# Kernel tuning notes

Hardware: AMD Instinct MI355X
Metric: run time of the kernel (lower is better)

## Reference

```python
import jax, jax.numpy as jnp
import numpy as np

N_QUBITS = 8
N_CYCLES = 4
B = 8192
C64 = jnp.complex64

# ---- gate matrices ----

def _ry_batched(t):  # t: [B] -> [B,2,2]
    c = jnp.cos(t / 2).astype(C64)
    s = jnp.sin(t / 2).astype(C64)
    return jnp.stack([jnp.stack([c, -s], -1), jnp.stack([s, c], -1)], -2)


def _rz_batched(p):  # p: [B] -> [B,2,2]
    e0 = jnp.exp(-0.5j * p.astype(C64))
    e1 = jnp.exp(0.5j * p.astype(C64))
    z = jnp.zeros_like(e0)
    return jnp.stack([jnp.stack([e0, z], -1), jnp.stack([z, e1], -1)], -2)


def _rx(t):  # scalar -> [2,2]
    c = jnp.cos(t / 2).astype(C64)
    s = (-1j * jnp.sin(t / 2)).astype(C64)
    return jnp.stack([jnp.stack([c, s]), jnp.stack([s, c])])


def _crx(t):  # scalar -> [4,4] block-diag(I2, RX(t)), control = first index
    return jnp.eye(4, dtype=C64).at[2:, 2:].set(_rx(t))


def _u3(t, p, l):  # scalars -> [2,2]
    ct = jnp.cos(t / 2).astype(C64)
    st = jnp.sin(t / 2).astype(C64)
    eil = jnp.exp(1j * l.astype(C64))
    eip = jnp.exp(1j * p.astype(C64))
    return jnp.stack([jnp.stack([ct, -eil * st]), jnp.stack([eip * st, eip * eil * ct])])

CNOT = jnp.array([[1, 0, 0, 0], [0, 1, 0, 0], [0, 0, 0, 1], [0, 0, 1, 0]], dtype=C64)

# ---- statevector ops (state: [B] + [2]*N_QUBITS) ----

def apply_1q(state, U, wire):
    b = state.shape[0]
    s = jnp.moveaxis(state, 1 + wire, 1).reshape(b, 2, -1)
    s = jnp.einsum('bij,bjk->bik', U, s) if U.ndim == 3 else jnp.einsum('ij,bjk->bik', U, s)
    return jnp.moveaxis(s.reshape((b,) + (2,) * N_QUBITS), 1, 1 + wire)


def apply_2q(state, U, wc, wt):
    b = state.shape[0]
    s = jnp.moveaxis(state, (1 + wc, 1 + wt), (1, 2)).reshape(b, 4, -1)
    s = jnp.einsum('ij,bjk->bik', U, s)
    return jnp.moveaxis(s.reshape((b,) + (2,) * N_QUBITS), (1, 2), (1 + wc, 1 + wt))


def expval_z(state, wire):  # <Z_wire> : [B]
    probs = state.real ** 2 + state.imag ** 2
    axes = tuple(a for a in range(1, N_QUBITS + 1) if a != 1 + wire)
    z = jnp.sum(probs, axis=axes)  # [B,2]
    return z[:, 0] - z[:, 1]


def _circuit(theta, phi, crx_params, u3_params):
    b = theta.shape[0]
    state = jnp.zeros((b, 2 ** N_QUBITS), dtype=C64).at[:, 0].set(1.0)
    state = state.reshape((b,) + (2,) * N_QUBITS)
    # circuit builder: RY(theta), RZ(phi) on every wire + CNOT ring, n_cycles times
    U = jnp.einsum('bij,bjk->bik', _rz_batched(phi), _ry_batched(theta))  # RZ @ RY, [B,2,2]
    for _ in range(N_CYCLES):
        for w in range(N_QUBITS):
            state = apply_1q(state, U, w)
        for w in range(N_QUBITS):
            state = apply_2q(state, CNOT, w, (w + 1) % N_QUBITS)
    # QCNN layer 1
    for i, (c, t) in enumerate([(0, 1), (2, 3), (4, 5), (6, 7), (1, 2), (3, 4), (5, 6)]):
        state = apply_2q(state, _crx(crx_params[i]), c, t)
    # (intermediate expvals on [0,2,4,6] are computed then discarded in original)
    for i, w in enumerate([1, 3, 5, 7]):
        p = u3_params[i]
        state = apply_1q(state, _u3(p[0], p[1], p[2]), w)
    for i, (c, t) in enumerate([(1, 3), (5, 7), (3, 5)]):
        state = apply_2q(state, _crx(crx_params[7 + i]), c, t)
    for i, w in enumerate([3, 7]):
        p = u3_params[4 + i]
        state = apply_1q(state, _u3(p[0], p[1], p[2]), w)
    state = apply_2q(state, _crx(crx_params[10]), 3, 7)
    p = u3_params[6]
    state = apply_1q(state, _u3(p[0], p[1], p[2]), 7)
    ev = expval_z(state, 7)[:, None]  # [B,1]
    return jax.nn.relu(ev)


def setup_inputs() -> dict:
    key = jax.random.key(0)
    k1, k2, k3, k4 = jax.random.split(key, 4)
    two_pi = 2.0 * np.pi
    return {
        'theta': jax.random.uniform(k1, (B,), jnp.float32, 0.0, two_pi),
        'phi': jax.random.uniform(k2, (B,), jnp.float32, 0.0, two_pi),
        'crx_params': jax.random.uniform(k3, (11,), jnp.float32, 0.0, two_pi),
        'u3_params': jax.random.uniform(k4, (7, 3), jnp.float32, 0.0, two_pi),
    }


def reference(theta, phi, crx_params, u3_params):
    return _circuit(theta, phi, crx_params, u3_params)
```

## Files before the change

kernel.cpp:

```cpp
#include <hip/hip_runtime.h>
#include <math.h>


typedef float v2f __attribute__((ext_vector_type(2)));

__device__ __forceinline__ v2f pkmul(v2f a, v2f b) {
  v2f d; asm("v_pk_mul_f32 %0, %1, %2" : "=v"(d) : "v"(a), "v"(b)); return d;
}
__device__ __forceinline__ v2f pkfma(v2f a, v2f b, v2f c) {
  v2f d; asm("v_pk_fma_f32 %0, %1, %2, %3" : "=v"(d) : "v"(a), "v"(b), "v"(c)); return d;
}
__device__ __forceinline__ v2f pkmul_lo1(v2f a, v2f b) {
  v2f d; asm("v_pk_mul_f32 %0, %1, %2 op_sel:[0,0] op_sel_hi:[1,0]"
             : "=v"(d) : "v"(a), "v"(b)); return d;
}
__device__ __forceinline__ v2f pkfma_lo1(v2f a, v2f b, v2f c) {
  v2f d; asm("v_pk_fma_f32 %0, %1, %2, %3 op_sel:[0,0,0] op_sel_hi:[1,0,1]"
             : "=v"(d) : "v"(a), "v"(b), "v"(c)); return d;
}
__device__ __forceinline__ v2f pkfma_hi1(v2f a, v2f b, v2f c) {
  v2f d; asm("v_pk_fma_f32 %0, %1, %2, %3 op_sel:[0,1,0] op_sel_hi:[1,1,1]"
             : "=v"(d) : "v"(a), "v"(b), "v"(c)); return d;
}
__device__ __forceinline__ v2f pkfma_sw1(v2f a, v2f b, v2f c) {
  v2f d; asm("v_pk_fma_f32 %0, %1, %2, %3 op_sel:[0,1,0] op_sel_hi:[1,0,1]"
             : "=v"(d) : "v"(a), "v"(b), "v"(c)); return d;
}
__device__ __forceinline__ v2f dup(float x) { return (v2f){x, x}; }

template <int M>
__device__ __forceinline__ float shxm(float v) {
  if constexpr (M == 1 || M == 2 || M == 3 || M == 7 || M == 8 || M == 15) {
    constexpr int ctrl = (M == 1) ? 0xB1 : (M == 2) ? 0x4E : (M == 3) ? 0x1B
                         : (M == 7) ? 0x141 : (M == 8) ? 0x128 : 0x140;
    return __int_as_float(__builtin_amdgcn_update_dpp(
        0, __float_as_int(v), ctrl, 0xF, 0xF, true));
  } else {
    return __int_as_float(__builtin_amdgcn_ds_swizzle(
        __float_as_int(v), (M << 10) | 0x1F));
  }
}
template <int M>
__device__ __forceinline__ v2f shf2(v2f a) {
  return (v2f){shxm<M>(a.x), shxm<M>(a.y)};
}

struct G1 { float r00, i00, r01, i01, r10, i10, r11, i11; };

__device__ __forceinline__ void cplx_fma(v2f& R, v2f& I, v2f PR, v2f PI,
                                         v2f cAr, v2f cAi, v2f cAiN,
                                         v2f cBr, v2f cBi, v2f cBiN) {
  v2f NR = pkfma(cBiN, PI, pkfma(cBr, PR, pkfma(cAiN, I, pkmul(cAr, R))));
  v2f NI = pkfma(cBi, PR, pkfma(cBr, PI, pkfma(cAi, R, pkmul(cAr, I))));
  R = NR; I = NI;
}

__device__ __forceinline__ void apply_pair(v2f& LR, v2f& LI, v2f& HR, v2f& HI,
                                           float g00r, float g00i, float g01r,
                                           float g01i, float g10r, float g10i,
                                           float g11r, float g11i) {
  const v2f a00r = dup(g00r), a00i = dup(g00i), n00i = dup(-g00i);
  const v2f a01r = dup(g01r), a01i = dup(g01i), n01i = dup(-g01i);
  const v2f a10r = dup(g10r), a10i = dup(g10i), n10i = dup(-g10i);
  const v2f a11r = dup(g11r), a11i = dup(g11i), n11i = dup(-g11i);
  v2f NLR = pkfma(n01i, HI, pkfma(a01r, HR, pkfma(n00i, LI, pkmul(a00r, LR))));
  v2f NLI = pkfma(a01i, HR, pkfma(a01r, HI, pkfma(a00i, LR, pkmul(a00r, LI))));
  v2f NHR = pkfma(n11i, HI, pkfma(a11r, HR, pkfma(n10i, LI, pkmul(a10r, LR))));
  v2f NHI = pkfma(a11i, HR, pkfma(a11r, HI, pkfma(a10i, LR, pkmul(a10r, LI))));
  LR = NLR; LI = NLI; HR = NHR; HI = NHI;
}

__device__ __forceinline__ void crx_pairv(v2f& LR, v2f& LI, v2f& HR, v2f& HI,
                                          v2f cCC, v2f cSS, v2f cSSN) {
  v2f NLR = pkfma(cSS, HI, pkmul(cCC, LR));
  v2f NLI = pkfma(cSSN, HR, pkmul(cCC, LI));
  v2f NHR = pkfma(cSS, LI, pkmul(cCC, HR));
  v2f NHI = pkfma(cSSN, LR, pkmul(cCC, HI));
  LR = NLR; LI = NLI; HR = NHR; HI = NHI;
}

template <int RL, int VL>
__device__ __forceinline__ void u_lane(v2f (&CR)[4], v2f (&CI)[4], int l,
                                       float uAr, float uBi, float uAip,
                                       float uBrp) {
  const bool hi = (__popc(l & RL) & 1) != 0;
  const float Ai = hi ? uAip : -uAip;
  const float Br = hi ? uBrp : -uBrp;
  const v2f cAr = dup(uAr), cAi = dup(Ai), cAiN = dup(-Ai);
  const v2f cBr = dup(Br), cBi = dup(uBi), cBiN = dup(-uBi);
  v2f PR[4], PI[4];
#pragma unroll
  for (int q = 0; q < 4; ++q) { PR[q] = shf2<VL>(CR[q]); PI[q] = shf2<VL>(CI[q]); }
#pragma unroll
  for (int q = 0; q < 4; ++q)
    cplx_fma(CR[q], CI[q], PR[q], PI[q], cAr, cAi, cAiN, cBr, cBi, cBiN);
}

__device__ __forceinline__ void gate_pack(v2f (&CR)[4], v2f (&CI)[4],
                                          v2f cA, v2f cB, v2f cBn,
                                          v2f cC, v2f cD, v2f cDn) {
#pragma unroll
  for (int q = 0; q < 4; ++q) {
    v2f NR = pkfma_hi1(cDn, CI[q], pkfma_hi1(cC, CR[q],
             pkfma_lo1(cBn, CI[q], pkmul_lo1(cA, CR[q]))));
    v2f NI = pkfma_hi1(cD, CR[q], pkfma_hi1(cC, CI[q],
             pkfma_lo1(cB, CR[q], pkmul_lo1(cA, CI[q]))));
    CR[q] = NR; CI[q] = NI;
  }
}

__device__ __forceinline__ void u_reg4(v2f (&CR)[4], v2f (&CI)[4], float uAr,
                                       float uBi, float uAip, float uBrp) {
  gate_pack(CR, CI,
            (v2f){uAr, uBrp},
            (v2f){-uAip, uBi},
            (v2f){uAip, -uBi},
            (v2f){-uBrp, uAr},
            (v2f){uBi, uAip},
            (v2f){-uBi, -uAip});
}

__device__ __forceinline__ void u3_reg4(v2f (&CR)[4], v2f (&CI)[4], const G1& g) {
  gate_pack(CR, CI,
            (v2f){g.r00, g.r10},
            (v2f){g.i00, g.i10},
            (v2f){-g.i00, -g.i10},
            (v2f){g.r01, g.r11},
            (v2f){g.i01, g.i11},
            (v2f){-g.i01, -g.i11});
}

template <int RL>
__device__ __forceinline__ void cnot_lr4(v2f (&CR)[4], v2f (&CI)[4], int l) {
  const bool c = (__popc(l & RL) & 1) != 0;
#pragma unroll
  for (int q = 0; q < 4; ++q) {
    const float ax = CR[q].x, ay = CR[q].y;
    CR[q] = (v2f){c ? ay : ax, c ? ax : ay};
    const float bx = CI[q].x, by = CI[q].y;
    CI[q] = (v2f){c ? by : bx, c ? bx : by};
  }
}

__device__ __forceinline__ void cnot_swap42(v2f (&CR)[4], v2f (&CI)[4]) {
  float t;
  t = CR[0].y; CR[0].y = CR[2].y; CR[2].y = t;
  t = CR[1].y; CR[1].y = CR[3].y; CR[3].y = t;
  t = CI[0].y; CI[0].y = CI[2].y; CI[2].y = t;
  t = CI[1].y; CI[1].y = CI[3].y; CI[3].y = t;
}

__device__ __forceinline__ void cnot_swap21(v2f (&CR)[4], v2f (&CI)[4]) {
  v2f t;
  t = CR[2]; CR[2] = CR[3]; CR[3] = t;
  t = CI[2]; CI[2] = CI[3]; CI[3] = t;
}

template <int VL>
__device__ __forceinline__ void cnot_rl(v2f (&CR)[4], v2f (&CI)[4]) {
  CR[1] = shf2<VL>(CR[1]); CI[1] = shf2<VL>(CI[1]);
  CR[3] = shf2<VL>(CR[3]); CI[3] = shf2<VL>(CI[3]);
}

template <int RL, int VL>
__device__ __forceinline__ void crx_ll(v2f (&CR)[4], v2f (&CI)[4], int l,
                                       float co, float si) {
  const bool c = (__popc(l & RL) & 1) != 0;
  const float cc = c ? co : 1.f, ss = c ? si : 0.f;
  const v2f cCC = dup(cc), cSS = dup(ss), cSSN = dup(-ss);
  v2f PR[4], PI[4];
#pragma unroll
  for (int q = 0; q < 4; ++q) { PR[q] = shf2<VL>(CR[q]); PI[q] = shf2<VL>(CI[q]); }
#pragma unroll
  for (int q = 0; q < 4; ++q) {
    CR[q] = pkfma(cSS, PI[q], pkmul(cCC, CR[q]));
    CI[q] = pkfma(cSSN, PR[q], pkmul(cCC, CI[q]));
  }
}

template <int RL>
__device__ __forceinline__ void crx_lr4(v2f (&CR)[4], v2f (&CI)[4], int l,
                                        float co, float si) {
  const bool c = (__popc(l & RL) & 1) != 0;
  const float cc = c ? co : 1.f, ss = c ? si : 0.f;
  const v2f cc2 = dup(cc), ss2 = dup(ss), ssN2 = dup(-ss);
#pragma unroll
  for (int q = 0; q < 4; ++q) {
    v2f NR = pkfma_sw1(ss2, CI[q], pkmul(cc2, CR[q]));
    v2f NI = pkfma_sw1(ssN2, CR[q], pkmul(cc2, CI[q]));
    CR[q] = NR; CI[q] = NI;
  }
}

template <int RL, int VL>
__device__ __forceinline__ void u3_lane(v2f (&CR)[4], v2f (&CI)[4], int l,
                                        const G1& g) {
  const bool hi = (__popc(l & RL) & 1) != 0;
  const float Ar = hi ? g.r11 : g.r00, Aii = hi ? g.i11 : g.i00;
  const float Br = hi ? g.r10 : g.r01, Bi = hi ? g.i10 : g.i01;
  const v2f cAr = dup(Ar), cAi = dup(Aii), cAiN = dup(-Aii);
  const v2f cBr = dup(Br), cBi = dup(Bi), cBiN = dup(-Bi);
  v2f PR[4], PI[4];
#pragma unroll
  for (int q = 0; q < 4; ++q) { PR[q] = shf2<VL>(CR[q]); PI[q] = shf2<VL>(CI[q]); }
#pragma unroll
  for (int q = 0; q < 4; ++q)
    cplx_fma(CR[q], CI[q], PR[q], PI[q], cAr, cAi, cAiN, cBr, cBi, cBiN);
}

__device__ __forceinline__ G1 load_g1(const float* __restrict__ cs, int k) {
  const float* p = cs + 22 + 8 * k;
  G1 g;
  g.r00 = p[0]; g.i00 = p[1]; g.r01 = p[2]; g.i01 = p[3];
  g.r10 = p[4]; g.i10 = p[5]; g.r11 = p[6]; g.i11 = p[7];
  return g;
}

__global__ void prep_kernel(const float* __restrict__ crx,
                            const float* __restrict__ u3p,
                            float* __restrict__ ws) {
  const int t = threadIdx.x;
  if (t < 11) {
    float s, c;
    sincosf(0.5f * crx[t], &s, &c);
    ws[2 * t] = c; ws[2 * t + 1] = s;
  } else if (t >= 16 && t < 23) {
    const int k = t - 16;
    float st, ct, sp, cp, sl, cl;
    sincosf(0.5f * u3p[3 * k], &st, &ct);
    sincosf(u3p[3 * k + 1], &sp, &cp);
    sincosf(u3p[3 * k + 2], &sl, &cl);
    float* o = ws + 22 + 8 * k;
    o[0] = ct;            o[1] = 0.f;
    o[2] = -cl * st;      o[3] = -sl * st;
    o[4] = cp * st;       o[5] = sp * st;
    o[6] = (cp * cl - sp * sl) * ct;
    o[7] = (sp * cl + cp * sl) * ct;
  }
}

__global__ __launch_bounds__(256, 4) void qcnn_kernel(
    const float* __restrict__ theta, const float* __restrict__ phi,
    const float* __restrict__ cs, float* __restrict__ out, int nbatch) {
  const int tid = blockIdx.x * blockDim.x + threadIdx.x;
  const int wave = tid >> 6;
  const int lane = threadIdx.x & 63;
  const int l = lane & 31;
  int b = wave * 2 + (lane >> 5);
  if (b >= nbatch) b = nbatch - 1;

  v2f CR[4], CI[4];
#pragma unroll
  for (int q = 0; q < 4; ++q) { CR[q] = dup(0.f); CI[q] = dup(0.f); }
  if (l == 0) CR[0].x = 1.f;

  const float th = theta[b], ph = phi[b];
  float sth, cth, sph, cph;
  __sincosf(0.5f * th, &sth, &cth);
  __sincosf(0.5f * ph, &sph, &cph);
  const float uAr = cph * cth, uBi = sph * sth;
  const float uAip = sph * cth, uBrp = cph * sth;

#define ULANE(RL, VL) u_lane<RL, VL>(CR, CI, l, uAr, uBi, uAip, uBrp)
#define UPAIR(a, b_) apply_pair(CR[a], CI[a], CR[b_], CI[b_], uAr, -uAip, \
                                -uBrp, uBi, uBrp, uBi, uAr, uAip)
#define UREGS() do { u_reg4(CR, CI, uAr, uBi, uAip, uBrp); \
                     UPAIR(0, 2); UPAIR(1, 3); \
                     UPAIR(0, 1); UPAIR(2, 3); } while (0)
#define RING(RL45, VL70) do { cnot_lr4<RL45>(CR, CI, l); \
                              cnot_swap42(CR, CI); cnot_swap21(CR, CI); \
                              cnot_rl<VL70>(CR, CI); } while (0)

  ULANE(16, 16); ULANE(8, 8);   ULANE(4, 4);   ULANE(2, 2);  ULANE(1, 1);
  UREGS(); RING(31, 24);
  ULANE(16, 24); ULANE(24, 12); ULANE(28, 6);  ULANE(30, 3); ULANE(31, 1);
  UREGS(); RING(21, 20);
  ULANE(16, 20); ULANE(8, 10);  ULANE(20, 5);  ULANE(10, 2); ULANE(21, 1);
  UREGS(); RING(19, 30);
  ULANE(16, 30); ULANE(24, 15); ULANE(12, 7);  ULANE(6, 3);  ULANE(19, 1);
  UREGS(); RING(17, 17);
#undef RING
#undef UREGS
#undef UPAIR
#undef ULANE

#define LD(k) const float co##k = cs[2 * k], si##k = cs[2 * k + 1]
  LD(0); crx_ll<16, 8>(CR, CI, l, co0, si0);
  LD(1); crx_ll<4, 2>(CR, CI, l, co1, si1);
  LD(2); crx_lr4<17>(CR, CI, l, co2, si2);
  LD(3);
  crx_pairv(CR[2], CI[2], CR[3], CI[3], dup(co3), dup(si3), dup(-si3));
  LD(4); crx_ll<8, 4>(CR, CI, l, co4, si4);
  LD(5); crx_ll<2, 1>(CR, CI, l, co5, si5);
  LD(6);
  {
    const v2f cCC = (v2f){1.f, co6}, cSS = (v2f){0.f, si6}, cSSN = (v2f){0.f, -si6};
    crx_pairv(CR[0], CI[0], CR[2], CI[2], cCC, cSS, cSSN);
    crx_pairv(CR[1], CI[1], CR[3], CI[3], cCC, cSS, cSSN);
  }

  { G1 g = load_g1(cs, 0); u3_lane<8, 8>(CR, CI, l, g); }
  { G1 g = load_g1(cs, 1); u3_lane<2, 2>(CR, CI, l, g); }
  { G1 g = load_g1(cs, 2); u3_reg4(CR, CI, g); }
  { G1 g = load_g1(cs, 3);
    apply_pair(CR[0], CI[0], CR[1], CI[1], g.r00, g.i00, g.r01, g.i01,
               g.r10, g.i10, g.r11, g.i11);
    apply_pair(CR[2], CI[2], CR[3], CI[3], g.r00, g.i00, g.r01, g.i01,
               g.r10, g.i10, g.r11, g.i11); }

  LD(7); crx_ll<8, 2>(CR, CI, l, co7, si7);
  LD(8);
  {
    const v2f cCC = (v2f){1.f, co8}, cSS = (v2f){0.f, si8}, cSSN = (v2f){0.f, -si8};
    crx_pairv(CR[0], CI[0], CR[1], CI[1], cCC, cSS, cSSN);
    crx_pairv(CR[2], CI[2], CR[3], CI[3], cCC, cSS, cSSN);
  }
  LD(9); crx_lr4<2>(CR, CI, l, co9, si9);

  { G1 g = load_g1(cs, 4); u3_lane<2, 2>(CR, CI, l, g); }
  { G1 g = load_g1(cs, 5);
    apply_pair(CR[0], CI[0], CR[1], CI[1], g.r00, g.i00, g.r01, g.i01,
               g.r10, g.i10, g.r11, g.i11);
    apply_pair(CR[2], CI[2], CR[3], CI[3], g.r00, g.i00, g.r01, g.i01,
               g.r10, g.i10, g.r11, g.i11); }

  LD(10);
  {
    const bool c = (__popc(l & 2) & 1) != 0;
    const float cc = c ? co10 : 1.f, ss = c ? si10 : 0.f;
    const v2f cCC = dup(cc), cSS = dup(ss), cSSN = dup(-ss);
    crx_pairv(CR[0], CI[0], CR[1], CI[1], cCC, cSS, cSSN);
    crx_pairv(CR[2], CI[2], CR[3], CI[3], cCC, cSS, cSSN);
  }

  { G1 g = load_g1(cs, 6);
    apply_pair(CR[0], CI[0], CR[1], CI[1], g.r00, g.i00, g.r01, g.i01,
               g.r10, g.i10, g.r11, g.i11);
    apply_pair(CR[2], CI[2], CR[3], CI[3], g.r00, g.i00, g.r01, g.i01,
               g.r10, g.i10, g.r11, g.i11); }
#undef LD

  v2f S0 = pkfma(CI[0], CI[0], pkmul(CR[0], CR[0]));
  v2f S1 = pkfma(CI[1], CI[1], pkmul(CR[1], CR[1]));
  v2f S2 = pkfma(CI[2], CI[2], pkmul(CR[2], CR[2]));
  v2f S3 = pkfma(CI[3], CI[3], pkmul(CR[3], CR[3]));
  const v2f T = (S0 + S2) - (S1 + S3);
  float v = T.x + T.y;
  v += shxm<1>(v); v += shxm<2>(v); v += shxm<4>(v);
  v += shxm<8>(v); v += shxm<16>(v);
  if (l == 0) out[b] = fmaxf(v, 0.f);
}

extern "C" void kernel_launch(void* const* d_in, const int* in_sizes, int n_in,
                              void* d_out, int out_size, void* d_ws, size_t ws_size,
                              hipStream_t stream) {
  const float* theta = (const float*)d_in[0];
  const float* phi = (const float*)d_in[1];
  const float* crx = (const float*)d_in[2];
  const float* u3p = (const float*)d_in[3];
  float* out = (float*)d_out;
  float* ws = (float*)d_ws;
  const int nb = in_sizes[0];

  prep_kernel<<<1, 64, 0, stream>>>(crx, u3p, ws);

  const int elems_per_block = 8;
  dim3 block(256);
  dim3 grid((nb + elems_per_block - 1) / elems_per_block);
  qcnn_kernel<<<grid, block, 0, stream>>>(theta, phi, ws, out, nb);
}
```

Measured before the change: 78.18 us.

## Map each batch element to a full 64-lane wave with 4 amplitudes per lane

Changes the statevector split so a whole wave64 holds one batch element, each lane keeping 4 complex amplitudes instead of 8 across a half-wave. Gates on the extra qubit now run across lanes, using __shfl_xor for the 32-lane distance. Hand-written packed-FMA inline asm is replaced by compiler builtins (elementwise fma, shufflevector). Launch bounds go to 8 waves per SIMD and blocks to 4 elements. The intent is lower register pressure and higher occupancy, paid for with more cross-lane shuffles, including a slower cross-half shuffle, and twice as many waves.

```diff
diff --git a/kernel.cpp b/kernel.cpp
--- a/kernel.cpp
+++ b/kernel.cpp
@@ -4,27 +4,11 @@
 
 typedef float v2f __attribute__((ext_vector_type(2)));
 
-__device__ __forceinline__ v2f pkmul(v2f a, v2f b) {
-  v2f d; asm("v_pk_mul_f32 %0, %1, %2" : "=v"(d) : "v"(a), "v"(b)); return d;
-}
-__device__ __forceinline__ v2f pkfma(v2f a, v2f b, v2f c) {
-  v2f d; asm("v_pk_fma_f32 %0, %1, %2, %3" : "=v"(d) : "v"(a), "v"(b), "v"(c)); return d;
-}
-__device__ __forceinline__ v2f pkmul_lo1(v2f a, v2f b) {
-  v2f d; asm("v_pk_mul_f32 %0, %1, %2 op_sel:[0,0] op_sel_hi:[1,0]"
-             : "=v"(d) : "v"(a), "v"(b)); return d;
-}
-__device__ __forceinline__ v2f pkfma_lo1(v2f a, v2f b, v2f c) {
-  v2f d; asm("v_pk_fma_f32 %0, %1, %2, %3 op_sel:[0,0,0] op_sel_hi:[1,0,1]"
-             : "=v"(d) : "v"(a), "v"(b), "v"(c)); return d;
-}
-__device__ __forceinline__ v2f pkfma_hi1(v2f a, v2f b, v2f c) {
-  v2f d; asm("v_pk_fma_f32 %0, %1, %2, %3 op_sel:[0,1,0] op_sel_hi:[1,1,1]"
-             : "=v"(d) : "v"(a), "v"(b), "v"(c)); return d;
-}
-__device__ __forceinline__ v2f pkfma_sw1(v2f a, v2f b, v2f c) {
-  v2f d; asm("v_pk_fma_f32 %0, %1, %2, %3 op_sel:[0,1,0] op_sel_hi:[1,0,1]"
-             : "=v"(d) : "v"(a), "v"(b), "v"(c)); return d;
+__device__ __forceinline__ v2f vfma(v2f a, v2f b, v2f c) {
+  return __builtin_elementwise_fma(a, b, c);
+}
+__device__ __forceinline__ v2f vswap(v2f a) {
+  return __builtin_shufflevector(a, a, 1, 0);
 }
 __device__ __forceinline__ v2f dup(float x) { return (v2f){x, x}; }
 
@@ -35,9 +19,11 @@
                          : (M == 7) ? 0x141 : (M == 8) ? 0x128 : 0x140;
     return __int_as_float(__builtin_amdgcn_update_dpp(
         0, __float_as_int(v), ctrl, 0xF, 0xF, true));
-  } else {
+  } else if constexpr (M < 32) {
     return __int_as_float(__builtin_amdgcn_ds_swizzle(
         __float_as_int(v), (M << 10) | 0x1F));
+  } else {
+    return __shfl_xor(v, M, 64);
   }
 }
 template <int M>
@@ -47,165 +33,123 @@
 
 struct G1 { float r00, i00, r01, i01, r10, i10, r11, i11; };
 
-__device__ __forceinline__ void cplx_fma(v2f& R, v2f& I, v2f PR, v2f PI,
-                                         v2f cAr, v2f cAi, v2f cAiN,
-                                         v2f cBr, v2f cBi, v2f cBiN) {
-  v2f NR = pkfma(cBiN, PI, pkfma(cBr, PR, pkfma(cAiN, I, pkmul(cAr, R))));
-  v2f NI = pkfma(cBi, PR, pkfma(cBr, PI, pkfma(cAi, R, pkmul(cAr, I))));
-  R = NR; I = NI;
-}
-
-__device__ __forceinline__ void apply_pair(v2f& LR, v2f& LI, v2f& HR, v2f& HI,
-                                           float g00r, float g00i, float g01r,
-                                           float g01i, float g10r, float g10i,
-                                           float g11r, float g11i) {
-  const v2f a00r = dup(g00r), a00i = dup(g00i), n00i = dup(-g00i);
-  const v2f a01r = dup(g01r), a01i = dup(g01i), n01i = dup(-g01i);
-  const v2f a10r = dup(g10r), a10i = dup(g10i), n10i = dup(-g10i);
-  const v2f a11r = dup(g11r), a11i = dup(g11i), n11i = dup(-g11i);
-  v2f NLR = pkfma(n01i, HI, pkfma(a01r, HR, pkfma(n00i, LI, pkmul(a00r, LR))));
-  v2f NLI = pkfma(a01i, HR, pkfma(a01r, HI, pkfma(a00i, LR, pkmul(a00r, LI))));
-  v2f NHR = pkfma(n11i, HI, pkfma(a11r, HR, pkfma(n10i, LI, pkmul(a10r, LR))));
-  v2f NHI = pkfma(a11i, HR, pkfma(a11r, HI, pkfma(a10i, LR, pkmul(a10r, LI))));
-  LR = NLR; LI = NLI; HR = NHR; HI = NHI;
-}
-
-__device__ __forceinline__ void crx_pairv(v2f& LR, v2f& LI, v2f& HR, v2f& HI,
-                                          v2f cCC, v2f cSS, v2f cSSN) {
-  v2f NLR = pkfma(cSS, HI, pkmul(cCC, LR));
-  v2f NLI = pkfma(cSSN, HR, pkmul(cCC, LI));
-  v2f NHR = pkfma(cSS, LI, pkmul(cCC, HR));
-  v2f NHI = pkfma(cSSN, LR, pkmul(cCC, HI));
-  LR = NLR; LI = NLI; HR = NHR; HI = NHI;
-}
-
 template <int RL, int VL>
-__device__ __forceinline__ void u_lane(v2f (&CR)[4], v2f (&CI)[4], int l,
+__device__ __forceinline__ void u_lane(v2f (&CR)[2], v2f (&CI)[2], int l,
                                        float uAr, float uBi, float uAip,
                                        float uBrp) {
   const bool hi = (__popc(l & RL) & 1) != 0;
-  const float Ai = hi ? uAip : -uAip;
-  const float Br = hi ? uBrp : -uBrp;
-  const v2f cAr = dup(uAr), cAi = dup(Ai), cAiN = dup(-Ai);
-  const v2f cBr = dup(Br), cBi = dup(uBi), cBiN = dup(-uBi);
-  v2f PR[4], PI[4];
-#pragma unroll
-  for (int q = 0; q < 4; ++q) { PR[q] = shf2<VL>(CR[q]); PI[q] = shf2<VL>(CI[q]); }
-#pragma unroll
-  for (int q = 0; q < 4; ++q)
-    cplx_fma(CR[q], CI[q], PR[q], PI[q], cAr, cAi, cAiN, cBr, cBi, cBiN);
-}
-
-__device__ __forceinline__ void gate_pack(v2f (&CR)[4], v2f (&CI)[4],
-                                          v2f cA, v2f cB, v2f cBn,
-                                          v2f cC, v2f cD, v2f cDn) {
-#pragma unroll
-  for (int q = 0; q < 4; ++q) {
-    v2f NR = pkfma_hi1(cDn, CI[q], pkfma_hi1(cC, CR[q],
-             pkfma_lo1(cBn, CI[q], pkmul_lo1(cA, CR[q]))));
-    v2f NI = pkfma_hi1(cD, CR[q], pkfma_hi1(cC, CI[q],
-             pkfma_lo1(cB, CR[q], pkmul_lo1(cA, CI[q]))));
+  const v2f cAr = dup(uAr), cBi = dup(uBi);
+  const v2f cAi = dup(hi ? uAip : -uAip);
+  const v2f cBr = dup(hi ? uBrp : -uBrp);
+  v2f PR[2], PI[2];
+#pragma unroll
+  for (int q = 0; q < 2; ++q) { PR[q] = shf2<VL>(CR[q]); PI[q] = shf2<VL>(CI[q]); }
+#pragma unroll
+  for (int q = 0; q < 2; ++q) {
+    v2f NR = vfma(-cBi, PI[q], vfma(cBr, PR[q], vfma(-cAi, CI[q], cAr * CR[q])));
+    v2f NI = vfma(cBi, PR[q], vfma(cBr, PI[q], vfma(cAi, CR[q], cAr * CI[q])));
     CR[q] = NR; CI[q] = NI;
   }
 }
 
-__device__ __forceinline__ void u_reg4(v2f (&CR)[4], v2f (&CI)[4], float uAr,
+__device__ __forceinline__ void u_pack(v2f (&CR)[2], v2f (&CI)[2], float uAr,
                                        float uBi, float uAip, float uBrp) {
-  gate_pack(CR, CI,
-            (v2f){uAr, uBrp},
-            (v2f){-uAip, uBi},
-            (v2f){uAip, -uBi},
-            (v2f){-uBrp, uAr},
-            (v2f){uBi, uAip},
-            (v2f){-uBi, -uAip});
-}
-
-__device__ __forceinline__ void u3_reg4(v2f (&CR)[4], v2f (&CI)[4], const G1& g) {
-  gate_pack(CR, CI,
-            (v2f){g.r00, g.r10},
-            (v2f){g.i00, g.i10},
-            (v2f){-g.i00, -g.i10},
-            (v2f){g.r01, g.r11},
-            (v2f){g.i01, g.i11},
-            (v2f){-g.i01, -g.i11});
+  const v2f Arv = dup(uAr), Biv = dup(uBi);
+  const v2f Aiv = (v2f){-uAip, uAip};
+  const v2f Brv = (v2f){-uBrp, uBrp};
+#pragma unroll
+  for (int q = 0; q < 2; ++q) {
+    const v2f XR = CR[q], XI = CI[q], SR = vswap(XR), SI = vswap(XI);
+    CR[q] = vfma(-Biv, SI, vfma(Brv, SR, vfma(-Aiv, XI, Arv * XR)));
+    CI[q] = vfma(Biv, SR, vfma(Brv, SI, vfma(Aiv, XR, Arv * XI)));
+  }
+}
+
+__device__ __forceinline__ void g_pair(v2f (&CR)[2], v2f (&CI)[2], float g00r,
+                                       float g00i, float g01r, float g01i,
+                                       float g10r, float g10i, float g11r,
+                                       float g11i) {
+  const v2f LR = CR[0], LI = CI[0], HR = CR[1], HI = CI[1];
+  CR[0] = vfma(dup(-g01i), HI, vfma(dup(g01r), HR, vfma(dup(-g00i), LI, dup(g00r) * LR)));
+  CI[0] = vfma(dup(g01i), HR, vfma(dup(g01r), HI, vfma(dup(g00i), LR, dup(g00r) * LI)));
+  CR[1] = vfma(dup(-g11i), HI, vfma(dup(g11r), HR, vfma(dup(-g10i), LI, dup(g10r) * LR)));
+  CI[1] = vfma(dup(g11i), HR, vfma(dup(g11r), HI, vfma(dup(g10i), LR, dup(g10r) * LI)));
 }
 
 template <int RL>
-__device__ __forceinline__ void cnot_lr4(v2f (&CR)[4], v2f (&CI)[4], int l) {
+__device__ __forceinline__ void cnot_l_pack(v2f (&CR)[2], v2f (&CI)[2], int l) {
   const bool c = (__popc(l & RL) & 1) != 0;
 #pragma unroll
-  for (int q = 0; q < 4; ++q) {
-    const float ax = CR[q].x, ay = CR[q].y;
-    CR[q] = (v2f){c ? ay : ax, c ? ax : ay};
-    const float bx = CI[q].x, by = CI[q].y;
-    CI[q] = (v2f){c ? by : bx, c ? bx : by};
-  }
-}
-
-__device__ __forceinline__ void cnot_swap42(v2f (&CR)[4], v2f (&CI)[4]) {
+  for (int q = 0; q < 2; ++q) {
+    const v2f r = CR[q], i = CI[q];
+    CR[q] = (v2f){c ? r.y : r.x, c ? r.x : r.y};
+    CI[q] = (v2f){c ? i.y : i.x, c ? i.x : i.y};
+  }
+}
+
+__device__ __forceinline__ void cnot_pack_bit0(v2f (&CR)[2], v2f (&CI)[2]) {
   float t;
-  t = CR[0].y; CR[0].y = CR[2].y; CR[2].y = t;
-  t = CR[1].y; CR[1].y = CR[3].y; CR[3].y = t;
-  t = CI[0].y; CI[0].y = CI[2].y; CI[2].y = t;
-  t = CI[1].y; CI[1].y = CI[3].y; CI[3].y = t;
-}
-
-__device__ __forceinline__ void cnot_swap21(v2f (&CR)[4], v2f (&CI)[4]) {
-  v2f t;
-  t = CR[2]; CR[2] = CR[3]; CR[3] = t;
-  t = CI[2]; CI[2] = CI[3]; CI[3] = t;
+  t = CR[0].y; CR[0].y = CR[1].y; CR[1].y = t;
+  t = CI[0].y; CI[0].y = CI[1].y; CI[1].y = t;
 }
 
 template <int VL>
-__device__ __forceinline__ void cnot_rl(v2f (&CR)[4], v2f (&CI)[4]) {
+__device__ __forceinline__ void cnot_bit0_lane(v2f (&CR)[2], v2f (&CI)[2]) {
   CR[1] = shf2<VL>(CR[1]); CI[1] = shf2<VL>(CI[1]);
-  CR[3] = shf2<VL>(CR[3]); CI[3] = shf2<VL>(CI[3]);
 }
 
 template <int RL, int VL>
-__device__ __forceinline__ void crx_ll(v2f (&CR)[4], v2f (&CI)[4], int l,
+__device__ __forceinline__ void crx_ll(v2f (&CR)[2], v2f (&CI)[2], int l,
                                        float co, float si) {
   const bool c = (__popc(l & RL) & 1) != 0;
-  const float cc = c ? co : 1.f, ss = c ? si : 0.f;
-  const v2f cCC = dup(cc), cSS = dup(ss), cSSN = dup(-ss);
-  v2f PR[4], PI[4];
-#pragma unroll
-  for (int q = 0; q < 4; ++q) { PR[q] = shf2<VL>(CR[q]); PI[q] = shf2<VL>(CI[q]); }
-#pragma unroll
-  for (int q = 0; q < 4; ++q) {
-    CR[q] = pkfma(cSS, PI[q], pkmul(cCC, CR[q]));
-    CI[q] = pkfma(cSSN, PR[q], pkmul(cCC, CI[q]));
+  const v2f cc = dup(c ? co : 1.f), ss = dup(c ? si : 0.f);
+  v2f PR[2], PI[2];
+#pragma unroll
+  for (int q = 0; q < 2; ++q) { PR[q] = shf2<VL>(CR[q]); PI[q] = shf2<VL>(CI[q]); }
+#pragma unroll
+  for (int q = 0; q < 2; ++q) {
+    CR[q] = vfma(ss, PI[q], cc * CR[q]);
+    CI[q] = vfma(-ss, PR[q], cc * CI[q]);
   }
 }
 
 template <int RL>
-__device__ __forceinline__ void crx_lr4(v2f (&CR)[4], v2f (&CI)[4], int l,
-                                        float co, float si) {
+__device__ __forceinline__ void crx_l_pack(v2f (&CR)[2], v2f (&CI)[2], int l,
+                                           float co, float si) {
   const bool c = (__popc(l & RL) & 1) != 0;
-  const float cc = c ? co : 1.f, ss = c ? si : 0.f;
-  const v2f cc2 = dup(cc), ss2 = dup(ss), ssN2 = dup(-ss);
-#pragma unroll
-  for (int q = 0; q < 4; ++q) {
-    v2f NR = pkfma_sw1(ss2, CI[q], pkmul(cc2, CR[q]));
-    v2f NI = pkfma_sw1(ssN2, CR[q], pkmul(cc2, CI[q]));
-    CR[q] = NR; CI[q] = NI;
-  }
+  const v2f cc = dup(c ? co : 1.f), ss = dup(c ? si : 0.f);
+#pragma unroll
+  for (int q = 0; q < 2; ++q) {
+    const v2f SR = vswap(CR[q]), SI = vswap(CI[q]);
+    CR[q] = vfma(ss, SI, cc * CR[q]);
+    CI[q] = vfma(-ss, SR, cc * CI[q]);
+  }
+}
+
+__device__ __forceinline__ void crx_pair(v2f (&CR)[2], v2f (&CI)[2], v2f cc,
+                                         v2f ss) {
+  const v2f LR = CR[0], LI = CI[0], HR = CR[1], HI = CI[1];
+  CR[0] = vfma(ss, HI, cc * LR);
+  CI[0] = vfma(-ss, HR, cc * LI);
+  CR[1] = vfma(ss, LI, cc * HR);
+  CI[1] = vfma(-ss, LR, cc * HI);
 }
 
 template <int RL, int VL>
-__device__ __forceinline__ void u3_lane(v2f (&CR)[4], v2f (&CI)[4], int l,
+__device__ __forceinline__ void u3_lane(v2f (&CR)[2], v2f (&CI)[2], int l,
                                         const G1& g) {
   const bool hi = (__popc(l & RL) & 1) != 0;
-  const float Ar = hi ? g.r11 : g.r00, Aii = hi ? g.i11 : g.i00;
-  const float Br = hi ? g.r10 : g.r01, Bi = hi ? g.i10 : g.i01;
-  const v2f cAr = dup(Ar), cAi = dup(Aii), cAiN = dup(-Aii);
-  const v2f cBr = dup(Br), cBi = dup(Bi), cBiN = dup(-Bi);
-  v2f PR[4], PI[4];
-#pragma unroll
-  for (int q = 0; q < 4; ++q) { PR[q] = shf2<VL>(CR[q]); PI[q] = shf2<VL>(CI[q]); }
-#pragma unroll
-  for (int q = 0; q < 4; ++q)
-    cplx_fma(CR[q], CI[q], PR[q], PI[q], cAr, cAi, cAiN, cBr, cBi, cBiN);
+  const v2f Ar = dup(hi ? g.r11 : g.r00), Ai = dup(hi ? g.i11 : g.i00);
+  const v2f Br = dup(hi ? g.r10 : g.r01), Bi = dup(hi ? g.i10 : g.i01);
+  v2f PR[2], PI[2];
+#pragma unroll
+  for (int q = 0; q < 2; ++q) { PR[q] = shf2<VL>(CR[q]); PI[q] = shf2<VL>(CI[q]); }
+#pragma unroll
+  for (int q = 0; q < 2; ++q) {
+    v2f NR = vfma(-Bi, PI[q], vfma(Br, PR[q], vfma(-Ai, CI[q], Ar * CR[q])));
+    v2f NI = vfma(Bi, PR[q], vfma(Br, PI[q], vfma(Ai, CR[q], Ar * CI[q])));
+    CR[q] = NR; CI[q] = NI;
+  }
 }
 
 __device__ __forceinline__ G1 load_g1(const float* __restrict__ cs, int k) {
@@ -239,116 +183,86 @@
   }
 }
 
-__global__ __launch_bounds__(256, 4) void qcnn_kernel(
+__global__ __launch_bounds__(256, 8) void qcnn_kernel(
     const float* __restrict__ theta, const float* __restrict__ phi,
     const float* __restrict__ cs, float* __restrict__ out, int nbatch) {
-  const int tid = blockIdx.x * blockDim.x + threadIdx.x;
-  const int wave = tid >> 6;
   const int lane = threadIdx.x & 63;
-  const int l = lane & 31;
-  int b = wave * 2 + (lane >> 5);
+  int b = blockIdx.x * 4 + (threadIdx.x >> 6);
   if (b >= nbatch) b = nbatch - 1;
 
-  v2f CR[4], CI[4];
-#pragma unroll
-  for (int q = 0; q < 4; ++q) { CR[q] = dup(0.f); CI[q] = dup(0.f); }
-  if (l == 0) CR[0].x = 1.f;
-
-  const float th = theta[b], ph = phi[b];
+  v2f CR[2], CI[2];
+  CR[0] = (v2f){lane == 0 ? 1.f : 0.f, 0.f};
+  CR[1] = dup(0.f); CI[0] = dup(0.f); CI[1] = dup(0.f);
+
   float sth, cth, sph, cph;
-  __sincosf(0.5f * th, &sth, &cth);
-  __sincosf(0.5f * ph, &sph, &cph);
+  __sincosf(0.5f * theta[b], &sth, &cth);
+  __sincosf(0.5f * phi[b], &sph, &cph);
   const float uAr = cph * cth, uBi = sph * sth;
   const float uAip = sph * cth, uBrp = cph * sth;
 
-#define ULANE(RL, VL) u_lane<RL, VL>(CR, CI, l, uAr, uBi, uAip, uBrp)
-#define UPAIR(a, b_) apply_pair(CR[a], CI[a], CR[b_], CI[b_], uAr, -uAip, \
-                                -uBrp, uBi, uBrp, uBi, uAr, uAip)
-#define UREGS() do { u_reg4(CR, CI, uAr, uBi, uAip, uBrp); \
-                     UPAIR(0, 2); UPAIR(1, 3); \
-                     UPAIR(0, 1); UPAIR(2, 3); } while (0)
-#define RING(RL45, VL70) do { cnot_lr4<RL45>(CR, CI, l); \
-                              cnot_swap42(CR, CI); cnot_swap21(CR, CI); \
-                              cnot_rl<VL70>(CR, CI); } while (0)
-
-  ULANE(16, 16); ULANE(8, 8);   ULANE(4, 4);   ULANE(2, 2);  ULANE(1, 1);
-  UREGS(); RING(31, 24);
-  ULANE(16, 24); ULANE(24, 12); ULANE(28, 6);  ULANE(30, 3); ULANE(31, 1);
-  UREGS(); RING(21, 20);
-  ULANE(16, 20); ULANE(8, 10);  ULANE(20, 5);  ULANE(10, 2); ULANE(21, 1);
-  UREGS(); RING(19, 30);
-  ULANE(16, 30); ULANE(24, 15); ULANE(12, 7);  ULANE(6, 3);  ULANE(19, 1);
-  UREGS(); RING(17, 17);
+#define UL(RL, VL) u_lane<RL, VL>(CR, CI, lane, uAr, uBi, uAip, uBrp)
+#define UREST() do { u_pack(CR, CI, uAr, uBi, uAip, uBrp); \
+                     g_pair(CR, CI, uAr, -uAip, -uBrp, uBi, \
+                            uBrp, uBi, uAr, uAip); } while (0)
+#define RING(RLC, VL70) do { cnot_l_pack<RLC>(CR, CI, lane); \
+                             cnot_pack_bit0(CR, CI); \
+                             cnot_bit0_lane<VL70>(CR, CI); } while (0)
+
+  UL(32, 32); UL(16, 16); UL(8, 8);   UL(4, 4);  UL(2, 2);  UL(1, 1);
+  UREST(); RING(63, 48);
+  UL(32, 48); UL(48, 24); UL(56, 12); UL(60, 6); UL(62, 3); UL(63, 1);
+  UREST(); RING(21, 40);
+  UL(32, 40); UL(16, 20); UL(40, 10); UL(20, 5); UL(42, 2); UL(21, 1);
+  UREST(); RING(51, 60);
+  UL(32, 60); UL(48, 30); UL(24, 15); UL(12, 7); UL(38, 3); UL(51, 1);
+  UREST(); RING(17, 34);
 #undef RING
-#undef UREGS
-#undef UPAIR
-#undef ULANE
+#undef UREST
+#undef UL
 
 #define LD(k) const float co##k = cs[2 * k], si##k = cs[2 * k + 1]
-  LD(0); crx_ll<16, 8>(CR, CI, l, co0, si0);
-  LD(1); crx_ll<4, 2>(CR, CI, l, co1, si1);
-  LD(2); crx_lr4<17>(CR, CI, l, co2, si2);
-  LD(3);
-  crx_pairv(CR[2], CI[2], CR[3], CI[3], dup(co3), dup(si3), dup(-si3));
-  LD(4); crx_ll<8, 4>(CR, CI, l, co4, si4);
-  LD(5); crx_ll<2, 1>(CR, CI, l, co5, si5);
-  LD(6);
-  {
-    const v2f cCC = (v2f){1.f, co6}, cSS = (v2f){0.f, si6}, cSSN = (v2f){0.f, -si6};
-    crx_pairv(CR[0], CI[0], CR[2], CI[2], cCC, cSS, cSSN);
-    crx_pairv(CR[1], CI[1], CR[3], CI[3], cCC, cSS, cSSN);
-  }
-
-  { G1 g = load_g1(cs, 0); u3_lane<8, 8>(CR, CI, l, g); }
-  { G1 g = load_g1(cs, 1); u3_lane<2, 2>(CR, CI, l, g); }
-  { G1 g = load_g1(cs, 2); u3_reg4(CR, CI, g); }
+  LD(0); crx_ll<32, 17>(CR, CI, lane, co0, si0);
+  LD(1); crx_ll<8, 4>(CR, CI, lane, co1, si1);
+  LD(2); crx_ll<34, 1>(CR, CI, lane, co2, si2);
+  LD(3); crx_pair(CR, CI, (v2f){1.f, co3}, (v2f){0.f, si3});
+  LD(4); crx_ll<16, 8>(CR, CI, lane, co4, si4);
+  LD(5); crx_ll<4, 2>(CR, CI, lane, co5, si5);
+  LD(6); crx_l_pack<17>(CR, CI, lane, co6, si6);
+
+  { G1 g = load_g1(cs, 0); u3_lane<16, 17>(CR, CI, lane, g); }
+  { G1 g = load_g1(cs, 1); u3_lane<4, 4>(CR, CI, lane, g); }
+  { G1 g = load_g1(cs, 2); u3_lane<17, 1>(CR, CI, lane, g); }
   { G1 g = load_g1(cs, 3);
-    apply_pair(CR[0], CI[0], CR[1], CI[1], g.r00, g.i00, g.r01, g.i01,
-               g.r10, g.i10, g.r11, g.i11);
-    apply_pair(CR[2], CI[2], CR[3], CI[3], g.r00, g.i00, g.r01, g.i01,
-               g.r10, g.i10, g.r11, g.i11); }
-
-  LD(7); crx_ll<8, 2>(CR, CI, l, co7, si7);
+    g_pair(CR, CI, g.r00, g.i00, g.r01, g.i01, g.r10, g.i10, g.r11, g.i11); }
+
+  LD(7); crx_ll<16, 4>(CR, CI, lane, co7, si7);
   LD(8);
   {
-    const v2f cCC = (v2f){1.f, co8}, cSS = (v2f){0.f, si8}, cSSN = (v2f){0.f, -si8};
-    crx_pairv(CR[0], CI[0], CR[1], CI[1], cCC, cSS, cSSN);
-    crx_pairv(CR[2], CI[2], CR[3], CI[3], cCC, cSS, cSSN);
-  }
-  LD(9); crx_lr4<2>(CR, CI, l, co9, si9);
-
-  { G1 g = load_g1(cs, 4); u3_lane<2, 2>(CR, CI, l, g); }
+    const bool c = (__popc(lane & 17) & 1) != 0;
+    crx_pair(CR, CI, dup(c ? co8 : 1.f), dup(c ? si8 : 0.f));
+  }
+  LD(9); crx_ll<4, 1>(CR, CI, lane, co9, si9);
+
+  { G1 g = load_g1(cs, 4); u3_lane<4, 4>(CR, CI, lane, g); }
   { G1 g = load_g1(cs, 5);
-    apply_pair(CR[0], CI[0], CR[1], CI[1], g.r00, g.i00, g.r01, g.i01,
-               g.r10, g.i10, g.r11, g.i11);
-    apply_pair(CR[2], CI[2], CR[3], CI[3], g.r00, g.i00, g.r01, g.i01,
-               g.r10, g.i10, g.r11, g.i11); }
+    g_pair(CR, CI, g.r00, g.i00, g.r01, g.i01, g.r10, g.i10, g.r11, g.i11); }
 
   LD(10);
   {
-    const bool c = (__popc(l & 2) & 1) != 0;
-    const float cc = c ? co10 : 1.f, ss = c ? si10 : 0.f;
-    const v2f cCC = dup(cc), cSS = dup(ss), cSSN = dup(-ss);
-    crx_pairv(CR[0], CI[0], CR[1], CI[1], cCC, cSS, cSSN);
-    crx_pairv(CR[2], CI[2], CR[3], CI[3], cCC, cSS, cSSN);
+    const bool c = (__popc(lane & 4) & 1) != 0;
+    crx_pair(CR, CI, dup(c ? co10 : 1.f), dup(c ? si10 : 0.f));
   }
 
   { G1 g = load_g1(cs, 6);
-    apply_pair(CR[0], CI[0], CR[1], CI[1], g.r00, g.i00, g.r01, g.i01,
-               g.r10, g.i10, g.r11, g.i11);
-    apply_pair(CR[2], CI[2], CR[3], CI[3], g.r00, g.i00, g.r01, g.i01,
-               g.r10, g.i10, g.r11, g.i11); }
+    g_pair(CR, CI, g.r00, g.i00, g.r01, g.i01, g.r10, g.i10, g.r11, g.i11); }
 #undef LD
 
-  v2f S0 = pkfma(CI[0], CI[0], pkmul(CR[0], CR[0]));
-  v2f S1 = pkfma(CI[1], CI[1], pkmul(CR[1], CR[1]));
-  v2f S2 = pkfma(CI[2], CI[2], pkmul(CR[2], CR[2]));
-  v2f S3 = pkfma(CI[3], CI[3], pkmul(CR[3], CR[3]));
-  const v2f T = (S0 + S2) - (S1 + S3);
+  const v2f T = vfma(CR[0], CR[0], CI[0] * CI[0])
+              - vfma(CR[1], CR[1], CI[1] * CI[1]);
   float v = T.x + T.y;
   v += shxm<1>(v); v += shxm<2>(v); v += shxm<4>(v);
-  v += shxm<8>(v); v += shxm<16>(v);
-  if (l == 0) out[b] = fmaxf(v, 0.f);
+  v += shxm<8>(v); v += shxm<16>(v); v += shxm<32>(v);
+  if (lane == 0) out[b] = fmaxf(v, 0.f);
 }
 
 extern "C" void kernel_launch(void* const* d_in, const int* in_sizes, int n_in,
@@ -364,7 +278,7 @@
 
   prep_kernel<<<1, 64, 0, stream>>>(crx, u3p, ws);
 
-  const int elems_per_block = 8;
+  const int elems_per_block = 4;
   dim3 block(256);
   dim3 grid((nb + elems_per_block - 1) / elems_per_block);
   qcnn_kernel<<<grid, block, 0, stream>>>(theta, phi, ws, out, nb);
```

Measured after the change: 79.25 us. No clear change (+1.4%).

## Initialize first layer as product state and fold trailing gates into observable

Applied to the files above, without the earlier changes.

The first RY/RZ layer acting on |0...0> is replaced by a closed-form product state: each amplitude is built from per-qubit factors, so five lane gates and the register gates of that layer go away. The last U3, CRX and U3 gates, which act only on wires 3 and 7, are folded into a Hermitian 2x2 observable computed once in the prep kernel, whose weights depend on the control bit. The final expectation then uses probabilities plus cross terms instead of applying those gates. This removes gate arithmetic per batch element at the cost of a more complex epilogue and extra precomputation.

```diff
diff --git a/kernel.cpp b/kernel.cpp
--- a/kernel.cpp
+++ b/kernel.cpp
@@ -46,14 +46,6 @@
 }
 
 struct G1 { float r00, i00, r01, i01, r10, i10, r11, i11; };
-
-__device__ __forceinline__ void cplx_fma(v2f& R, v2f& I, v2f PR, v2f PI,
-                                         v2f cAr, v2f cAi, v2f cAiN,
-                                         v2f cBr, v2f cBi, v2f cBiN) {
-  v2f NR = pkfma(cBiN, PI, pkfma(cBr, PR, pkfma(cAiN, I, pkmul(cAr, R))));
-  v2f NI = pkfma(cBi, PR, pkfma(cBr, PI, pkfma(cAi, R, pkmul(cAr, I))));
-  R = NR; I = NI;
-}
 
 __device__ __forceinline__ void apply_pair(v2f& LR, v2f& LI, v2f& HR, v2f& HI,
                                            float g00r, float g00i, float g01r,
@@ -92,8 +84,11 @@
 #pragma unroll
   for (int q = 0; q < 4; ++q) { PR[q] = shf2<VL>(CR[q]); PI[q] = shf2<VL>(CI[q]); }
 #pragma unroll
-  for (int q = 0; q < 4; ++q)
-    cplx_fma(CR[q], CI[q], PR[q], PI[q], cAr, cAi, cAiN, cBr, cBi, cBiN);
+  for (int q = 0; q < 4; ++q) {
+    v2f NR = pkfma(cBiN, PI[q], pkfma(cBr, PR[q], pkfma(cAiN, CI[q], pkmul(cAr, CR[q]))));
+    v2f NI = pkfma(cBi, PR[q], pkfma(cBr, PI[q], pkfma(cAi, CR[q], pkmul(cAr, CI[q]))));
+    CR[q] = NR; CI[q] = NI;
+  }
 }
 
 __device__ __forceinline__ void gate_pack(v2f (&CR)[4], v2f (&CI)[4],
@@ -112,22 +107,14 @@
 __device__ __forceinline__ void u_reg4(v2f (&CR)[4], v2f (&CI)[4], float uAr,
                                        float uBi, float uAip, float uBrp) {
   gate_pack(CR, CI,
-            (v2f){uAr, uBrp},
-            (v2f){-uAip, uBi},
-            (v2f){uAip, -uBi},
-            (v2f){-uBrp, uAr},
-            (v2f){uBi, uAip},
-            (v2f){-uBi, -uAip});
+            (v2f){uAr, uBrp}, (v2f){-uAip, uBi}, (v2f){uAip, -uBi},
+            (v2f){-uBrp, uAr}, (v2f){uBi, uAip}, (v2f){-uBi, -uAip});
 }
 
 __device__ __forceinline__ void u3_reg4(v2f (&CR)[4], v2f (&CI)[4], const G1& g) {
   gate_pack(CR, CI,
-            (v2f){g.r00, g.r10},
-            (v2f){g.i00, g.i10},
-            (v2f){-g.i00, -g.i10},
-            (v2f){g.r01, g.r11},
-            (v2f){g.i01, g.i11},
-            (v2f){-g.i01, -g.i11});
+            (v2f){g.r00, g.r10}, (v2f){g.i00, g.i10}, (v2f){-g.i00, -g.i10},
+            (v2f){g.r01, g.r11}, (v2f){g.i01, g.i11}, (v2f){-g.i01, -g.i11});
 }
 
 template <int RL>
@@ -204,8 +191,11 @@
 #pragma unroll
   for (int q = 0; q < 4; ++q) { PR[q] = shf2<VL>(CR[q]); PI[q] = shf2<VL>(CI[q]); }
 #pragma unroll
-  for (int q = 0; q < 4; ++q)
-    cplx_fma(CR[q], CI[q], PR[q], PI[q], cAr, cAi, cAiN, cBr, cBi, cBiN);
+  for (int q = 0; q < 4; ++q) {
+    v2f NR = pkfma(cBiN, PI[q], pkfma(cBr, PR[q], pkfma(cAiN, CI[q], pkmul(cAr, CR[q]))));
+    v2f NI = pkfma(cBi, PR[q], pkfma(cBr, PI[q], pkfma(cAi, CR[q], pkmul(cAr, CI[q]))));
+    CR[q] = NR; CI[q] = NI;
+  }
 }
 
 __device__ __forceinline__ G1 load_g1(const float* __restrict__ cs, int k) {
@@ -214,6 +204,38 @@
   g.r00 = p[0]; g.i00 = p[1]; g.r01 = p[2]; g.i01 = p[3];
   g.r10 = p[4]; g.i10 = p[5]; g.r11 = p[6]; g.i11 = p[7];
   return g;
+}
+
+struct Cx { float r, i; };
+__device__ __forceinline__ Cx cmul(Cx a, Cx b) {
+  return {a.r * b.r - a.i * b.i, a.r * b.i + a.i * b.r};
+}
+__device__ __forceinline__ Cx cconj(Cx a) { return {a.r, -a.i}; }
+__device__ __forceinline__ Cx cadd(Cx a, Cx b) { return {a.r + b.r, a.i + b.i}; }
+__device__ __forceinline__ Cx csub(Cx a, Cx b) { return {a.r - b.r, a.i - b.i}; }
+__device__ __forceinline__ Cx cscale(float s, Cx a) { return {s * a.r, s * a.i}; }
+
+__device__ void congr(float n00, Cx n01, float n11, Cx G00, Cx G01, Cx G10,
+                      Cx G11, float& m00, Cx& m01, float& m11) {
+  Cx t0 = cadd(cscale(n00, G00), cmul(n01, G10));
+  Cx t1 = cadd(cmul(cconj(n01), G00), cscale(n11, G10));
+  Cx u0 = cadd(cscale(n00, G01), cmul(n01, G11));
+  Cx u1 = cadd(cmul(cconj(n01), G01), cscale(n11, G11));
+  m00 = cadd(cmul(cconj(G00), t0), cmul(cconj(G10), t1)).r;
+  m01 = cadd(cmul(cconj(G00), u0), cmul(cconj(G10), u1));
+  m11 = cadd(cmul(cconj(G01), u0), cmul(cconj(G11), u1)).r;
+}
+
+__device__ void build_u3(float t, float p, float l, Cx& G00, Cx& G01, Cx& G10,
+                         Cx& G11) {
+  float st, ct, sp, cp, sl, cl;
+  sincosf(0.5f * t, &st, &ct);
+  sincosf(p, &sp, &cp);
+  sincosf(l, &sl, &cl);
+  G00 = {ct, 0.f};
+  G01 = {-cl * st, -sl * st};
+  G10 = {cp * st, sp * st};
+  G11 = {(cp * cl - sp * sl) * ct, (sp * cl + cp * sl) * ct};
 }
 
 __global__ void prep_kernel(const float* __restrict__ crx,
@@ -236,6 +258,23 @@
     o[4] = cp * st;       o[5] = sp * st;
     o[6] = (cp * cl - sp * sl) * ct;
     o[7] = (sp * cl + cp * sl) * ct;
+  } else if (t == 30) {
+    Cx A00, A01, A10, A11, C00, C01, C10, C11;
+    build_u3(u3p[15], u3p[16], u3p[17], A00, A01, A10, A11);
+    build_u3(u3p[18], u3p[19], u3p[20], C00, C01, C10, C11);
+    float n00 = (C00.r * C00.r + C00.i * C00.i) - (C10.r * C10.r + C10.i * C10.i);
+    Cx n01 = csub(cmul(cconj(C00), C01), cmul(cconj(C10), C11));
+    float n11 = (C01.r * C01.r + C01.i * C01.i) - (C11.r * C11.r + C11.i * C11.i);
+    float m00, m11; Cx m01;
+    congr(n00, n01, n11, A00, A01, A10, A11, m00, m01, m11);
+    ws[80] = m00; ws[81] = m11; ws[82] = 2.f * m01.r; ws[83] = -2.f * m01.i;
+    float co, si;
+    sincosf(0.5f * crx[10], &si, &co);
+    Cx R00 = {co, 0.f}, R01 = {0.f, -si}, R10 = {0.f, -si}, R11 = {co, 0.f};
+    float p00, p11; Cx p01;
+    congr(n00, n01, n11, R00, R01, R10, R11, p00, p01, p11);
+    congr(p00, p01, p11, A00, A01, A10, A11, m00, m01, m11);
+    ws[84] = m00; ws[85] = m11; ws[86] = 2.f * m01.r; ws[87] = -2.f * m01.i;
   }
 }
 
@@ -249,30 +288,56 @@
   int b = wave * 2 + (lane >> 5);
   if (b >= nbatch) b = nbatch - 1;
 
-  v2f CR[4], CI[4];
-#pragma unroll
-  for (int q = 0; q < 4; ++q) { CR[q] = dup(0.f); CI[q] = dup(0.f); }
-  if (l == 0) CR[0].x = 1.f;
-
-  const float th = theta[b], ph = phi[b];
   float sth, cth, sph, cph;
-  __sincosf(0.5f * th, &sth, &cth);
-  __sincosf(0.5f * ph, &sph, &cph);
+  __sincosf(0.5f * theta[b], &sth, &cth);
+  __sincosf(0.5f * phi[b], &sph, &cph);
   const float uAr = cph * cth, uBi = sph * sth;
   const float uAip = sph * cth, uBrp = cph * sth;
 
+  const float g0r = uAr, g0i = -uAip, g1r = uBrp, g1i = uBi;
+  float Zr = (l & 16) ? g1r : g0r, Zi = (l & 16) ? g1i : g0i;
+#define MULBIT(m)                                                     \
+  {                                                                   \
+    const float Fr = (l & m) ? g1r : g0r, Fi = (l & m) ? g1i : g0i;   \
+    const float nr = Zr * Fr - Zi * Fi, ni = Zr * Fi + Zi * Fr;       \
+    Zr = nr; Zi = ni;                                                 \
+  }
+  MULBIT(8) MULBIT(4) MULBIT(2) MULBIT(1)
+#undef MULBIT
+  const float g00r = g0r * g0r - g0i * g0i, g00i = 2.f * g0r * g0i;
+  const float g11r = g1r * g1r - g1i * g1i, g11i = 2.f * g1r * g1i;
+  const float h0r = g00r * g0r - g00i * g0i, h0i = g00r * g0i + g00i * g0r;
+  const float h1r = g00r * g1r - g00i * g1i, h1i = g00r * g1i + g00i * g1r;
+  const float h2r = g11r * g0r - g11i * g0i, h2i = g11r * g0i + g11i * g0r;
+  const float h3r = g11r * g1r - g11i * g1i, h3i = g11r * g1i + g11i * g1r;
+
+  v2f CR[4], CI[4];
+  {
+    const v2f Zrv = dup(Zr), Ziv = dup(Zi), ZivN = dup(-Zi);
+    const v2f Hr[4] = {{h0r, h1r}, {h1r, h2r}, {h1r, h2r}, {h2r, h3r}};
+    const v2f Hi[4] = {{h0i, h1i}, {h1i, h2i}, {h1i, h2i}, {h2i, h3i}};
+#pragma unroll
+    for (int q = 0; q < 4; ++q) {
+      CR[q] = pkfma(ZivN, Hi[q], pkmul(Zrv, Hr[q]));
+      CI[q] = pkfma(Ziv, Hr[q], pkmul(Zrv, Hi[q]));
+    }
+  }
+
 #define ULANE(RL, VL) u_lane<RL, VL>(CR, CI, l, uAr, uBi, uAip, uBrp)
-#define UPAIR(a, b_) apply_pair(CR[a], CI[a], CR[b_], CI[b_], uAr, -uAip, \
-                                -uBrp, uBi, uBrp, uBi, uAr, uAip)
 #define UREGS() do { u_reg4(CR, CI, uAr, uBi, uAip, uBrp); \
-                     UPAIR(0, 2); UPAIR(1, 3); \
-                     UPAIR(0, 1); UPAIR(2, 3); } while (0)
+                     apply_pair(CR[0], CI[0], CR[2], CI[2], uAr, -uAip, \
+                                -uBrp, uBi, uBrp, uBi, uAr, uAip); \
+                     apply_pair(CR[1], CI[1], CR[3], CI[3], uAr, -uAip, \
+                                -uBrp, uBi, uBrp, uBi, uAr, uAip); \
+                     apply_pair(CR[0], CI[0], CR[1], CI[1], uAr, -uAip, \
+                                -uBrp, uBi, uBrp, uBi, uAr, uAip); \
+                     apply_pair(CR[2], CI[2], CR[3], CI[3], uAr, -uAip, \
+                                -uBrp, uBi, uBrp, uBi, uAr, uAip); } while (0)
 #define RING(RL45, VL70) do { cnot_lr4<RL45>(CR, CI, l); \
                               cnot_swap42(CR, CI); cnot_swap21(CR, CI); \
                               cnot_rl<VL70>(CR, CI); } while (0)
 
-  ULANE(16, 16); ULANE(8, 8);   ULANE(4, 4);   ULANE(2, 2);  ULANE(1, 1);
-  UREGS(); RING(31, 24);
+  RING(31, 24);
   ULANE(16, 24); ULANE(24, 12); ULANE(28, 6);  ULANE(30, 3); ULANE(31, 1);
   UREGS(); RING(21, 20);
   ULANE(16, 20); ULANE(8, 10);  ULANE(20, 5);  ULANE(10, 2); ULANE(21, 1);
@@ -281,7 +346,6 @@
   UREGS(); RING(17, 17);
 #undef RING
 #undef UREGS
-#undef UPAIR
 #undef ULANE
 
 #define LD(k) const float co##k = cs[2 * k], si##k = cs[2 * k + 1]
@@ -318,37 +382,29 @@
   LD(9); crx_lr4<2>(CR, CI, l, co9, si9);
 
   { G1 g = load_g1(cs, 4); u3_lane<2, 2>(CR, CI, l, g); }
-  { G1 g = load_g1(cs, 5);
-    apply_pair(CR[0], CI[0], CR[1], CI[1], g.r00, g.i00, g.r01, g.i01,
-               g.r10, g.i10, g.r11, g.i11);
-    apply_pair(CR[2], CI[2], CR[3], CI[3], g.r00, g.i00, g.r01, g.i01,
-               g.r10, g.i10, g.r11, g.i11); }
-
-  LD(10);
+#undef LD
+
   {
-    const bool c = (__popc(l & 2) & 1) != 0;
-    const float cc = c ? co10 : 1.f, ss = c ? si10 : 0.f;
-    const v2f cCC = dup(cc), cSS = dup(ss), cSSN = dup(-ss);
-    crx_pairv(CR[0], CI[0], CR[1], CI[1], cCC, cSS, cSSN);
-    crx_pairv(CR[2], CI[2], CR[3], CI[3], cCC, cSS, cSSN);
-  }
-
-  { G1 g = load_g1(cs, 6);
-    apply_pair(CR[0], CI[0], CR[1], CI[1], g.r00, g.i00, g.r01, g.i01,
-               g.r10, g.i10, g.r11, g.i11);
-    apply_pair(CR[2], CI[2], CR[3], CI[3], g.r00, g.i00, g.r01, g.i01,
-               g.r10, g.i10, g.r11, g.i11); }
-#undef LD
-
-  v2f S0 = pkfma(CI[0], CI[0], pkmul(CR[0], CR[0]));
-  v2f S1 = pkfma(CI[1], CI[1], pkmul(CR[1], CR[1]));
-  v2f S2 = pkfma(CI[2], CI[2], pkmul(CR[2], CR[2]));
-  v2f S3 = pkfma(CI[3], CI[3], pkmul(CR[3], CR[3]));
-  const v2f T = (S0 + S2) - (S1 + S3);
-  float v = T.x + T.y;
-  v += shxm<1>(v); v += shxm<2>(v); v += shxm<4>(v);
-  v += shxm<8>(v); v += shxm<16>(v);
-  if (l == 0) out[b] = fmaxf(v, 0.f);
+    const bool cH = (l & 2) != 0;
+    const float w00 = cH ? cs[84] : cs[80];
+    const float w11 = cH ? cs[85] : cs[81];
+    const float wa  = cH ? cs[86] : cs[82];
+    const float wb  = cH ? cs[87] : cs[83];
+    v2f PL = pkfma(CI[0], CI[0], pkmul(CR[0], CR[0]));
+    PL = PL + pkfma(CI[2], CI[2], pkmul(CR[2], CR[2]));
+    v2f PH = pkfma(CI[1], CI[1], pkmul(CR[1], CR[1]));
+    PH = PH + pkfma(CI[3], CI[3], pkmul(CR[3], CR[3]));
+    v2f X = pkfma(CI[0], CI[1], pkmul(CR[0], CR[1]));
+    X = X + pkfma(CI[2], CI[3], pkmul(CR[2], CR[3]));
+    v2f Y = pkmul(CR[0], CI[1]) - pkmul(CI[0], CR[1]);
+    Y = Y + (pkmul(CR[2], CI[3]) - pkmul(CI[2], CR[3]));
+    v2f EV = pkfma(dup(wb), Y, pkfma(dup(wa), X,
+             pkfma(dup(w11), PH, pkmul(dup(w00), PL))));
+    float v = EV.x + EV.y;
+    v += shxm<1>(v); v += shxm<2>(v); v += shxm<4>(v);
+    v += shxm<8>(v); v += shxm<16>(v);
+    if (l == 0) out[b] = fmaxf(v, 0.f);
+  }
 }
 
 extern "C" void kernel_launch(void* const* d_in, const int* in_sizes, int n_in,
```

After: 75.69 us (median of 2 runs). 1.03x faster.
